# Kernel tuning notes

Hardware: AMD Instinct MI355X
Metric: run time of the kernel (lower is better)

## Reference

```python
import jax, jax.numpy as jnp
import numpy as np

B, S, D, H = 2, 4096, 512, 8
DH = D // H

def setup_inputs() -> dict:
    key = jax.random.key(0)
    k_enc, kq, kk, kv, ko = jax.random.split(key, 5)
    xavier = float(np.sqrt(6.0 / (D + D)))
    enc = jax.random.normal(k_enc, (B, S, D), dtype=jnp.float32)
    W_Q = jax.random.uniform(kq, (D, D), jnp.float32, -xavier, xavier)
    W_K = jax.random.uniform(kk, (D, D), jnp.float32, -xavier, xavier)
    W_V = jax.random.uniform(kv, (D, D), jnp.float32, -xavier, xavier)
    W_O = jax.random.uniform(ko, (D, D), jnp.float32, -xavier, xavier)
    # lower-triangular causal mask, broadcast over batch and heads
    causal_mask = jnp.tril(jnp.ones((S, S), dtype=jnp.int32))[None, None]
    return {"enc": enc, "causal_mask": causal_mask,
            "W_Q": W_Q, "W_K": W_K, "W_V": W_V, "W_O": W_O}

def reference(enc, causal_mask, W_Q, W_K, W_V, W_O):
    b, s, _ = enc.shape
    q = (enc @ W_Q).reshape(b, s, H, DH).transpose(0, 2, 1, 3)  # [b,h,s,dh]
    k = (enc @ W_K).reshape(b, s, H, DH).transpose(0, 2, 1, 3)
    v = (enc @ W_V).reshape(b, s, H, DH).transpose(0, 2, 1, 3)
    scores = jnp.einsum('bhqd,bhkd->bhqk', q, k) / jnp.sqrt(jnp.float32(DH))
    scores = jnp.where(causal_mask == 0, -jnp.inf, scores)
    attn = jax.nn.softmax(scores, axis=-1)
    out = jnp.einsum('bhqk,bhkd->bhqd', attn, v)  # [b,h,s,dh]
    concat = out.transpose(0, 2, 1, 3).reshape(b, s, H * DH)
    return concat @ W_O
```

## Files before the change

kernel.cpp:

```cpp
#include <hip/hip_runtime.h>


typedef _Float16 f16x8 __attribute__((ext_vector_type(8)));
typedef float f32x16 __attribute__((ext_vector_type(16)));

__device__ __forceinline__ f32x16 mma32(f16x8 a, f16x8 b, f32x16 c) {
  return __builtin_amdgcn_mfma_f32_32x32x16_f16(a, b, c, 0, 0, 0);
}

__device__ __forceinline__ void gload16(const void* g, void* l) {
  __builtin_amdgcn_global_load_lds((const __attribute__((address_space(1))) void*)g,
                                   (__attribute__((address_space(3))) void*)l, 16, 0, 0);
}

__global__ __launch_bounds__(256) void prep_k(const float* __restrict__ enc,
                                              const float* __restrict__ WQ,
                                              const float* __restrict__ WK,
                                              const float* __restrict__ WV,
                                              const float* __restrict__ WO,
                                              _Float16* __restrict__ enc16,
                                              _Float16* __restrict__ WtQ,
                                              _Float16* __restrict__ WtK,
                                              _Float16* __restrict__ WtV,
                                              _Float16* __restrict__ WtO) {
  const int bid = blockIdx.x;
  if (bid < 2048) {
    const size_t i = (size_t)bid * 256 + threadIdx.x;
    const float4* p = (const float4*)(enc + i * 8);
    const float4 a = p[0], b = p[1];
    union { f16x8 v; uint4 u; } r;
    r.v[0] = (_Float16)a.x; r.v[1] = (_Float16)a.y; r.v[2] = (_Float16)a.z; r.v[3] = (_Float16)a.w;
    r.v[4] = (_Float16)b.x; r.v[5] = (_Float16)b.y; r.v[6] = (_Float16)b.z; r.v[7] = (_Float16)b.w;
    *(uint4*)(enc16 + i * 8) = r.u;
  } else {
    const int t = bid - 2048;
    const int wsel = t >> 8;
    const float* W = (wsel == 0) ? WQ : (wsel == 1) ? WK : (wsel == 2) ? WV : WO;
    _Float16* T = (wsel == 0) ? WtQ : (wsel == 1) ? WtK : (wsel == 2) ? WtV : WtO;
    const int tb = t & 255;
    const int k0 = (tb & 15) * 32, n0 = (tb >> 4) * 32;
    __shared__ float tt[32][33];
    const int c = threadIdx.x & 31, r8 = threadIdx.x >> 5;
#pragma unroll
    for (int p = 0; p < 4; ++p) tt[c][r8 + 8 * p] = W[(size_t)(k0 + r8 + 8 * p) * 512 + n0 + c];
    __syncthreads();
#pragma unroll
    for (int p = 0; p < 4; ++p)
      T[(size_t)(n0 + r8 + 8 * p) * 512 + k0 + c] = (_Float16)tt[r8 + 8 * p][c];
  }
}

__device__ __forceinline__ void gemm_core(const _Float16* __restrict__ A,
                                          const _Float16* __restrict__ Wt,
                                          int m0, int n0,
                                          _Float16* Al, _Float16* Bl,
                                          f32x16 acc[2][2]) {
  const int tid = threadIdx.x, w = tid >> 6, l = tid & 63;
  const int hi = l >> 5, li = l & 31;
  const int wm = w >> 1, wn = w & 1;
  const int srow = l >> 3, sunit = (l & 7) ^ (l >> 3);
  const int arow = 32 * w;

#pragma unroll
  for (int mb = 0; mb < 2; ++mb)
#pragma unroll
    for (int nb = 0; nb < 2; ++nb)
#pragma unroll
      for (int r = 0; r < 16; ++r) acc[mb][nb][r] = 0.f;

#pragma unroll
  for (int i = 0; i < 4; ++i) {
    gload16(A + (size_t)(m0 + arow + 8 * i + srow) * 512 + sunit * 8, Al + (arow + 8 * i) * 64);
    gload16(Wt + (size_t)(n0 + arow + 8 * i + srow) * 512 + sunit * 8, Bl + (arow + 8 * i) * 64);
  }
  for (int kk = 0; kk < 8; ++kk) {
    const int cur = kk & 1;
    __syncthreads();
    if (kk < 7) {
      const int kn = (kk + 1) * 64;
#pragma unroll
      for (int i = 0; i < 4; ++i) {
        gload16(A + (size_t)(m0 + arow + 8 * i + srow) * 512 + kn + sunit * 8,
                Al + (cur ^ 1) * 8192 + (arow + 8 * i) * 64);
        gload16(Wt + (size_t)(n0 + arow + 8 * i + srow) * 512 + kn + sunit * 8,
                Bl + (cur ^ 1) * 8192 + (arow + 8 * i) * 64);
      }
    }
#pragma unroll
    for (int ks = 0; ks < 4; ++ks) {
      f16x8 af[2], bf[2];
#pragma unroll
      for (int mb = 0; mb < 2; ++mb)
        af[mb] = *(const f16x8*)((const char*)(Al + cur * 8192 + (64 * wm + 32 * mb + li) * 64) +
                                 (((2 * ks + hi) ^ (li & 7)) << 4));
#pragma unroll
      for (int nb = 0; nb < 2; ++nb)
        bf[nb] = *(const f16x8*)((const char*)(Bl + cur * 8192 + (64 * wn + 32 * nb + li) * 64) +
                                 (((2 * ks + hi) ^ (li & 7)) << 4));
#pragma unroll
      for (int mb = 0; mb < 2; ++mb)
#pragma unroll
        for (int nb = 0; nb < 2; ++nb) acc[mb][nb] = mma32(af[mb], bf[nb], acc[mb][nb]);
    }
  }
}

__global__ __launch_bounds__(256) void qkv_k(const _Float16* __restrict__ A,
                                             const _Float16* __restrict__ WtQ,
                                             const _Float16* __restrict__ WtK,
                                             const _Float16* __restrict__ WtV,
                                             _Float16* __restrict__ Qw,
                                             _Float16* __restrict__ Kw,
                                             _Float16* __restrict__ Vpw,
                                             float qscale) {
  __shared__ __align__(16) _Float16 Al[2 * 128 * 64];
  __shared__ __align__(16) _Float16 Bl[2 * 128 * 64];
  const int m0 = blockIdx.x * 128;
  const int wid = blockIdx.y >> 2, n0 = (blockIdx.y & 3) * 128;
  const _Float16* Wt = (wid == 0) ? WtQ : (wid == 1) ? WtK : WtV;
  f32x16 acc[2][2];
  gemm_core(A, Wt, m0, n0, Al, Bl, acc);

  const int tid = threadIdx.x, w = tid >> 6, l = tid & 63;
  const int hi = l >> 5, li = l & 31;
  const int wm = w >> 1, wn = w & 1;
  if (wid < 2) {
    _Float16* Cp = (wid == 0) ? Qw : Kw;
    const float scale = (wid == 0) ? qscale : 1.f;
#pragma unroll
    for (int mb = 0; mb < 2; ++mb)
#pragma unroll
      for (int nb = 0; nb < 2; ++nb)
#pragma unroll
        for (int r = 0; r < 16; ++r) {
          const int m = m0 + 64 * wm + 32 * mb + (r & 3) + 8 * (r >> 2) + 4 * hi;
          const int n = n0 + 64 * wn + 32 * nb + li;
          const int b = m >> 12, s = m & 4095, h = n >> 6, d = n & 63;
          Cp[((((size_t)b * 8 + h) * 4096 + s) << 6) + d] = (_Float16)(acc[mb][nb][r] * scale);
        }
  } else {
#pragma unroll
    for (int mb = 0; mb < 2; ++mb)
#pragma unroll
      for (int nb = 0; nb < 2; ++nb)
#pragma unroll
        for (int c = 0; c < 4; ++c) {
          const int mbase = m0 + 64 * wm + 32 * mb + 16 * (c >> 1);
          const int n = n0 + 64 * wn + 32 * nb + li;
          const int b = mbase >> 12, sb = mbase & 4095, h = n >> 6, d = n & 63;
          union { uint2 u; _Float16 h4[4]; } t4;
#pragma unroll
          for (int t = 0; t < 4; ++t) t4.h4[t] = (_Float16)acc[mb][nb][4 * c + t];
          *(uint2*)(Vpw + ((((size_t)b * 8 + h) * 64 + d) << 12) + sb + 4 * (c & 1) + 8 * hi) = t4.u;
        }
  }
}

__global__ __launch_bounds__(256) void fgemm_k(const _Float16* __restrict__ A,
                                               const _Float16* __restrict__ Wt,
                                               float* __restrict__ out) {
  __shared__ __align__(16) _Float16 Al[2 * 128 * 64];
  __shared__ __align__(16) _Float16 Bl[2 * 128 * 64];
  const int m0 = blockIdx.x * 128, n0 = blockIdx.y * 128;
  f32x16 acc[2][2];
  gemm_core(A, Wt, m0, n0, Al, Bl, acc);
  const int tid = threadIdx.x, w = tid >> 6, l = tid & 63;
  const int hi = l >> 5, li = l & 31;
  const int wm = w >> 1, wn = w & 1;
#pragma unroll
  for (int mb = 0; mb < 2; ++mb)
#pragma unroll
    for (int nb = 0; nb < 2; ++nb)
#pragma unroll
      for (int r = 0; r < 16; ++r) {
        const int m = m0 + 64 * wm + 32 * mb + (r & 3) + 8 * (r >> 2) + 4 * hi;
        const int n = n0 + 64 * wn + 32 * nb + li;
        out[(size_t)m * 512 + n] = acc[mb][nb][r];
      }
}

__global__ __launch_bounds__(128) void flash_k(const _Float16* __restrict__ Q,
                                               const _Float16* __restrict__ K,
                                               const _Float16* __restrict__ Vp,
                                               _Float16* __restrict__ att,
                                               _Float16* __restrict__ pO,
                                               float2* __restrict__ ml) {
  __shared__ __align__(16) _Float16 Kl[2 * 64 * 64];
  __shared__ __align__(16) _Float16 Vl[2 * 64 * 64];

  const int u = blockIdx.x;
  const int bh = u & 15;
  const int j = u >> 4;
  int qt, ktlo, kthi, cc;
  if (j < 32) {
    qt = 32 + j; ktlo = 0; kthi = 31; cc = 0;
  } else {
    const int i = (j - 32) >> 1;
    qt = ((j - 32) & 1) ? 63 - i : 31 - i;
    ktlo = (qt >= 32) ? 32 : 0;
    kthi = qt; cc = 1;
  }
  const bool split = (qt >= 32);
  const int q0 = qt * 64;
  const int tid = threadIdx.x, w = tid >> 6, l = tid & 63;
  const int hi = l >> 5, li = l & 31;
  const int srow = l >> 3, sunit = (l & 7) ^ (l >> 3);

  const size_t bhoff = (size_t)bh * 4096 * 64;
  const _Float16* Kb = K + bhoff;
  const _Float16* Vb = Vp + bhoff;
  const _Float16* Qb = Q + bhoff;
  const int qg = q0 + 32 * w + li;

  f16x8 qB[4];
#pragma unroll
  for (int ks = 0; ks < 4; ++ks)
    qB[ks] = *(const f16x8*)(Qb + (size_t)qg * 64 + 16 * ks + 8 * hi);

  f32x16 o2[2], lacc;
#pragma unroll
  for (int db = 0; db < 2; ++db)
#pragma unroll
    for (int r = 0; r < 16; ++r) o2[db][r] = 0.f;
#pragma unroll
  for (int r = 0; r < 16; ++r) lacc[r] = 0.f;
  float m_ = -__builtin_inff();

#pragma unroll
  for (int e = 0; e < 4; ++e) {
    const int row = 32 * w + 8 * e;
    gload16(Kb + (size_t)(ktlo * 64 + row + srow) * 64 + sunit * 8, Kl + row * 64);
    gload16(Vb + (size_t)(row + srow) * 4096 + ktlo * 64 + sunit * 8, Vl + row * 64);
  }

  for (int kt = ktlo; kt <= kthi; ++kt) {
    const int cur = kt & 1;
    __syncthreads();
    if (kt < kthi) {
      const int k0n = (kt + 1) * 64;
#pragma unroll
      for (int e = 0; e < 4; ++e) {
        const int row = 32 * w + 8 * e;
        gload16(Kb + (size_t)(k0n + row + srow) * 64 + sunit * 8,
                Kl + (cur ^ 1) * 4096 + row * 64);
        gload16(Vb + (size_t)(row + srow) * 4096 + k0n + sunit * 8,
                Vl + (cur ^ 1) * 4096 + row * 64);
      }
    }

    f32x16 s2[2];
#pragma unroll
    for (int kb = 0; kb < 2; ++kb)
#pragma unroll
      for (int r = 0; r < 16; ++r) s2[kb][r] = 0.f;
    __builtin_amdgcn_s_setprio(1);
#pragma unroll
    for (int ks = 0; ks < 4; ++ks)
#pragma unroll
      for (int kb = 0; kb < 2; ++kb) {
        const f16x8 kf = *(const f16x8*)((const char*)(Kl + cur * 4096 + (32 * kb + li) * 64) +
                                         (((2 * ks + hi) ^ (li & 7)) << 4));
        s2[kb] = mma32(kf, qB[ks], s2[kb]);
      }
    __builtin_amdgcn_s_setprio(0);

    if (kt == qt) {
      const int limit = 32 * w + li;
#pragma unroll
      for (int kb = 0; kb < 2; ++kb)
#pragma unroll
        for (int r = 0; r < 16; ++r) {
          const int kl = 32 * kb + (r & 3) + 8 * (r >> 2) + 4 * hi;
          if (kl > limit) s2[kb][r] = -__builtin_inff();
        }
    }

#define RV(i) s2[(i) >> 4][(i) & 15]
    float a[11];
#pragma unroll
    for (int i = 0; i < 10; ++i)
      a[i] = fmaxf(fmaxf(RV(3 * i), RV(3 * i + 1)), RV(3 * i + 2));
    a[10] = fmaxf(RV(30), RV(31));
#undef RV
    float b4[4];
    b4[0] = fmaxf(fmaxf(a[0], a[1]), a[2]);
    b4[1] = fmaxf(fmaxf(a[3], a[4]), a[5]);
    b4[2] = fmaxf(fmaxf(a[6], a[7]), a[8]);
    b4[3] = fmaxf(a[9], a[10]);
    const float mxl = fmaxf(fmaxf(fmaxf(b4[0], b4[1]), b4[2]), b4[3]);

    if (!__all(mxl <= m_ + 8.f)) {
      const float vm = fmaxf(mxl, __shfl_xor(mxl, 32, 64));
      const float mn = fmaxf(m_, vm);
      const float al = __builtin_amdgcn_exp2f(m_ - mn);
      m_ = mn;
#pragma unroll
      for (int r = 0; r < 16; ++r) lacc[r] *= al;
#pragma unroll
      for (int db = 0; db < 2; ++db)
#pragma unroll
        for (int r = 0; r < 16; ++r) o2[db][r] *= al;
    }
#pragma unroll
    for (int kb = 0; kb < 2; ++kb)
#pragma unroll
      for (int r = 0; r < 16; ++r) s2[kb][r] = __builtin_amdgcn_exp2f(s2[kb][r] - m_);
#pragma unroll
    for (int kb = 0; kb < 2; ++kb)
#pragma unroll
      for (int r = 0; r < 16; ++r) lacc[r] += s2[kb][r];

    f16x8 pb[4];
#pragma unroll
    for (int ks = 0; ks < 4; ++ks) {
      union { f16x8 v; unsigned int u[4]; } pu;
      const int kb = ks >> 1, base = 8 * (ks & 1);
#pragma unroll
      for (int p2 = 0; p2 < 4; ++p2)
        pu.u[p2] = __builtin_bit_cast(unsigned int,
                     __builtin_amdgcn_cvt_pkrtz(s2[kb][base + 2 * p2], s2[kb][base + 2 * p2 + 1]));
      pb[ks] = pu.v;
    }

    __builtin_amdgcn_s_setprio(1);
#pragma unroll
    for (int ks = 0; ks < 4; ++ks)
#pragma unroll
      for (int db = 0; db < 2; ++db) {
        const f16x8 vf = *(const f16x8*)((const char*)(Vl + cur * 4096 + (32 * db + li) * 64) +
                                         (((2 * ks + hi) ^ (li & 7)) << 4));
        o2[db] = mma32(vf, pb[ks], o2[db]);
      }
    __builtin_amdgcn_s_setprio(0);
  }

  float t8[8];
#pragma unroll
  for (int i = 0; i < 8; ++i) t8[i] = lacc[i] + lacc[i + 8];
  float lsum = ((t8[0] + t8[1]) + (t8[2] + t8[3])) + ((t8[4] + t8[5]) + (t8[6] + t8[7]));
  lsum += __shfl_xor(lsum, 32, 64);
  const float inv = 1.f / lsum;
  if (!split) {
    const int b = bh >> 3, h = bh & 7;
    _Float16* op = att + ((size_t)b * 4096 + qg) * 512 + h * 64;
#pragma unroll
    for (int db = 0; db < 2; ++db)
#pragma unroll
      for (int c = 0; c < 4; ++c) {
        union { uint2 u; _Float16 h4[4]; } t4;
#pragma unroll
        for (int t = 0; t < 4; ++t) t4.h4[t] = (_Float16)(o2[db][4 * c + t] * inv);
        *(uint2*)(op + 32 * db + 8 * c + 4 * hi) = t4.u;
      }
  } else {
    const int slot = (bh * 32 + (qt - 32)) * 2 + cc;
    const int qrow = 32 * w + li;
    _Float16* op = pO + (size_t)slot * 4096 + qrow * 64;
#pragma unroll
    for (int db = 0; db < 2; ++db)
#pragma unroll
      for (int c = 0; c < 4; ++c) {
        union { uint2 u; _Float16 h4[4]; } t4;
#pragma unroll
        for (int t = 0; t < 4; ++t) t4.h4[t] = (_Float16)(o2[db][4 * c + t] * inv);
        *(uint2*)(op + 32 * db + 8 * c + 4 * hi) = t4.u;
      }
    if (hi == 0) ml[slot * 64 + qrow] = make_float2(m_, lsum);
  }
}

__global__ __launch_bounds__(256) void combine_k(const float2* __restrict__ ml,
                                                 const _Float16* __restrict__ pO,
                                                 _Float16* __restrict__ att) {
  const int tid = threadIdx.x;
  const int rid = blockIdx.x * 8 + (tid >> 5);
  const int d2 = tid & 31;
  const int bh = rid >> 11, rem = rid & 2047;
  const int qm = rem >> 6, qrow = rem & 63;
  const int slot0 = (bh * 32 + qm) * 2;
  const float2 ml0 = ml[slot0 * 64 + qrow];
  const float2 ml1 = ml[slot0 * 64 + 64 + qrow];
  const float M = fmaxf(ml0.x, ml1.x);
  const float w0 = __builtin_amdgcn_exp2f(ml0.x - M) * ml0.y;
  const float w1 = __builtin_amdgcn_exp2f(ml1.x - M) * ml1.y;
  const float inv = 1.f / (w0 + w1);
  const float a0 = w0 * inv, a1 = w1 * inv;
  union { unsigned int u; _Float16 h2[2]; } x0, x1, y;
  x0.u = *(const unsigned int*)(pO + (size_t)slot0 * 4096 + qrow * 64 + 2 * d2);
  x1.u = *(const unsigned int*)(pO + (size_t)(slot0 + 1) * 4096 + qrow * 64 + 2 * d2);
  y.h2[0] = (_Float16)((float)x0.h2[0] * a0 + (float)x1.h2[0] * a1);
  y.h2[1] = (_Float16)((float)x0.h2[1] * a0 + (float)x1.h2[1] * a1);
  const int b = bh >> 3, h = bh & 7, q = (32 + qm) * 64 + qrow;
  *(unsigned int*)(att + ((size_t)b * 4096 + q) * 512 + h * 64 + 2 * d2) = y.u;
}

extern "C" void kernel_launch(void* const* d_in, const int* in_sizes, int n_in,
                              void* d_out, int out_size, void* d_ws, size_t ws_size,
                              hipStream_t stream) {
  const float* enc = (const float*)d_in[0];
  const float* WQ = (const float*)d_in[2];
  const float* WK = (const float*)d_in[3];
  const float* WV = (const float*)d_in[4];
  const float* WO = (const float*)d_in[5];
  float* out = (float*)d_out;

  const size_t NE = (size_t)2 * 8 * 4096 * 64;
  _Float16* enc16 = (_Float16*)d_ws;
  _Float16* pO = enc16;
  _Float16* Qw = enc16 + NE;
  _Float16* Kw = Qw + NE;
  _Float16* Vpw = Kw + NE;
  _Float16* WtQ = Vpw + NE;
  _Float16* WtK = WtQ + 512 * 512;
  _Float16* WtV = WtK + 512 * 512;
  _Float16* WtO = WtV + 512 * 512;
  _Float16* att = WtO + 512 * 512;
  float2* ml = (float2*)WtQ;

  prep_k<<<3072, 256, 0, stream>>>(enc, WQ, WK, WV, WO, enc16, WtQ, WtK, WtV, WtO);
  qkv_k<<<dim3(64, 12), 256, 0, stream>>>(enc16, WtQ, WtK, WtV, Qw, Kw, Vpw, 0.1803368801f);
  flash_k<<<1536, 128, 0, stream>>>(Qw, Kw, Vpw, att, pO, ml);
  combine_k<<<4096, 256, 0, stream>>>(ml, pO, att);
  fgemm_k<<<dim3(64, 4), 256, 0, stream>>>(att, WtO, out);
}
```

Before: 111.9 us.

## Split causal flash attention into 20-tile KV chunks with heaviest-first scheduling

Replaces the two-way KV split of upper query tiles with chunks of up to 20 key tiles, so long query tiles are split into 2-4 partial blocks and the grid grows from 1536 to 2176 blocks, issued in reverse order so the largest work starts first. The combine kernel is generalised to merge a variable number of partials with log-sum-exp weights. Partial outputs are moved into the output buffer and the row statistics into the enc16 workspace to make room for more slots. This aims to even out per-block work and reduce tail imbalance, at the cost of more partial writes and combine traffic.

```diff
diff --git a/kernel.cpp b/kernel.cpp
--- a/kernel.cpp
+++ b/kernel.cpp
@@ -190,17 +190,15 @@
 
   const int u = blockIdx.x;
   const int bh = u & 15;
-  const int j = u >> 4;
-  int qt, ktlo, kthi, cc;
-  if (j < 32) {
-    qt = 32 + j; ktlo = 0; kthi = 31; cc = 0;
-  } else {
-    const int i = (j - 32) >> 1;
-    qt = ((j - 32) & 1) ? 63 - i : 31 - i;
-    ktlo = (qt >= 32) ? 32 : 0;
-    kthi = qt; cc = 1;
-  }
-  const bool split = (qt >= 32);
+  const int j = 135 - (u >> 4);
+  int qt, cc;
+  if (j < 20) { qt = j; cc = 0; }
+  else if (j < 60) { qt = 20 + ((j - 20) >> 1); cc = (j - 20) & 1; }
+  else if (j < 120) { qt = 40 + (j - 60) / 3; cc = (j - 60) % 3; }
+  else { qt = 60 + ((j - 120) >> 2); cc = (j - 120) & 3; }
+  const int ktlo = 20 * cc;
+  const int kthi = min(20 * cc + 19, qt);
+  const bool split = (qt >= 20);
   const int q0 = qt * 64;
   const int tid = threadIdx.x, w = tid >> 6, l = tid & 63;
   const int hi = l >> 5, li = l & 31;
@@ -353,7 +351,11 @@
         *(uint2*)(op + 32 * db + 8 * c + 4 * hi) = t4.u;
       }
   } else {
-    const int slot = (bh * 32 + (qt - 32)) * 2 + cc;
+    int off;
+    if (qt < 40) off = (qt - 20) * 2;
+    else if (qt < 60) off = 40 + (qt - 40) * 3;
+    else off = 100 + (qt - 60) * 4;
+    const int slot = bh * 116 + off + cc;
     const int qrow = 32 * w + li;
     _Float16* op = pO + (size_t)slot * 4096 + qrow * 64;
 #pragma unroll
@@ -375,22 +377,45 @@
   const int tid = threadIdx.x;
   const int rid = blockIdx.x * 8 + (tid >> 5);
   const int d2 = tid & 31;
-  const int bh = rid >> 11, rem = rid & 2047;
-  const int qm = rem >> 6, qrow = rem & 63;
-  const int slot0 = (bh * 32 + qm) * 2;
-  const float2 ml0 = ml[slot0 * 64 + qrow];
-  const float2 ml1 = ml[slot0 * 64 + 64 + qrow];
-  const float M = fmaxf(ml0.x, ml1.x);
-  const float w0 = __builtin_amdgcn_exp2f(ml0.x - M) * ml0.y;
-  const float w1 = __builtin_amdgcn_exp2f(ml1.x - M) * ml1.y;
-  const float inv = 1.f / (w0 + w1);
-  const float a0 = w0 * inv, a1 = w1 * inv;
-  union { unsigned int u; _Float16 h2[2]; } x0, x1, y;
-  x0.u = *(const unsigned int*)(pO + (size_t)slot0 * 4096 + qrow * 64 + 2 * d2);
-  x1.u = *(const unsigned int*)(pO + (size_t)(slot0 + 1) * 4096 + qrow * 64 + 2 * d2);
-  y.h2[0] = (_Float16)((float)x0.h2[0] * a0 + (float)x1.h2[0] * a1);
-  y.h2[1] = (_Float16)((float)x0.h2[1] * a0 + (float)x1.h2[1] * a1);
-  const int b = bh >> 3, h = bh & 7, q = (32 + qm) * 64 + qrow;
+  const int bh = rid / 2816, rem = rid % 2816;
+  const int qt = 20 + (rem >> 6), qrow = rem & 63;
+  const int nc = (qt + 20) / 20;
+  int off;
+  if (qt < 40) off = (qt - 20) * 2;
+  else if (qt < 60) off = 40 + (qt - 40) * 3;
+  else off = 100 + (qt - 60) * 4;
+  const int slot0 = bh * 116 + off;
+
+  float2 mlc[4];
+  float M = -__builtin_inff();
+#pragma unroll
+  for (int c = 0; c < 4; ++c)
+    if (c < nc) {
+      mlc[c] = ml[(slot0 + c) * 64 + qrow];
+      M = fmaxf(M, mlc[c].x);
+    }
+  float wc[4], wsum = 0.f;
+#pragma unroll
+  for (int c = 0; c < 4; ++c)
+    if (c < nc) {
+      wc[c] = __builtin_amdgcn_exp2f(mlc[c].x - M) * mlc[c].y;
+      wsum += wc[c];
+    }
+  const float inv = 1.f / wsum;
+  float acc0 = 0.f, acc1 = 0.f;
+#pragma unroll
+  for (int c = 0; c < 4; ++c)
+    if (c < nc) {
+      union { unsigned int u; _Float16 h2[2]; } x;
+      x.u = *(const unsigned int*)(pO + (size_t)(slot0 + c) * 4096 + qrow * 64 + 2 * d2);
+      const float a = wc[c] * inv;
+      acc0 += (float)x.h2[0] * a;
+      acc1 += (float)x.h2[1] * a;
+    }
+  union { unsigned int u; _Float16 h2[2]; } y;
+  y.h2[0] = (_Float16)acc0;
+  y.h2[1] = (_Float16)acc1;
+  const int b = bh >> 3, h = bh & 7, q = qt * 64 + qrow;
   *(unsigned int*)(att + ((size_t)b * 4096 + q) * 512 + h * 64 + 2 * d2) = y.u;
 }
 
@@ -406,7 +431,6 @@
 
   const size_t NE = (size_t)2 * 8 * 4096 * 64;
   _Float16* enc16 = (_Float16*)d_ws;
-  _Float16* pO = enc16;
   _Float16* Qw = enc16 + NE;
   _Float16* Kw = Qw + NE;
   _Float16* Vpw = Kw + NE;
@@ -415,11 +439,12 @@
   _Float16* WtV = WtK + 512 * 512;
   _Float16* WtO = WtV + 512 * 512;
   _Float16* att = WtO + 512 * 512;
-  float2* ml = (float2*)WtQ;
+  float2* ml = (float2*)enc16;
+  _Float16* pO = (_Float16*)d_out;
 
   prep_k<<<3072, 256, 0, stream>>>(enc, WQ, WK, WV, WO, enc16, WtQ, WtK, WtV, WtO);
   qkv_k<<<dim3(64, 12), 256, 0, stream>>>(enc16, WtQ, WtK, WtV, Qw, Kw, Vpw, 0.1803368801f);
-  flash_k<<<1536, 128, 0, stream>>>(Qw, Kw, Vpw, att, pO, ml);
-  combine_k<<<4096, 256, 0, stream>>>(ml, pO, att);
+  flash_k<<<2176, 128, 0, stream>>>(Qw, Kw, Vpw, att, pO, ml);
+  combine_k<<<5632, 256, 0, stream>>>(ml, pO, att);
   fgemm_k<<<dim3(64, 4), 256, 0, stream>>>(att, WtO, out);
 }
```

Measured after the change: 128.0 us. 1.14x slower.

## Load K/V in 128-key pairs per barrier, dropping double-buffer prefetch

Applied to the files above, without the earlier changes.

The flash attention kernel now loads two 64-key K/V tiles at once into a single 128-key LDS buffer, with a new swizzle for the wider V rows. It then processes both tiles between barriers. This halves the number of barrier rounds per key range. However, it removes the prefetch of the next tile that overlapped with compute, so every load is now exposed and waited on before any math runs.

```diff
diff --git a/kernel.cpp b/kernel.cpp
--- a/kernel.cpp
+++ b/kernel.cpp
@@ -185,8 +185,8 @@
                                                _Float16* __restrict__ att,
                                                _Float16* __restrict__ pO,
                                                float2* __restrict__ ml) {
-  __shared__ __align__(16) _Float16 Kl[2 * 64 * 64];
-  __shared__ __align__(16) _Float16 Vl[2 * 64 * 64];
+  __shared__ __align__(16) _Float16 Kl[128 * 64];
+  __shared__ __align__(16) _Float16 Vl[64 * 128];
 
   const int u = blockIdx.x;
   const int bh = u & 15;
@@ -204,7 +204,6 @@
   const int q0 = qt * 64;
   const int tid = threadIdx.x, w = tid >> 6, l = tid & 63;
   const int hi = l >> 5, li = l & 31;
-  const int srow = l >> 3, sunit = (l & 7) ^ (l >> 3);
 
   const size_t bhoff = (size_t)bh * 4096 * 64;
   const _Float16* Kb = K + bhoff;
@@ -226,28 +225,7 @@
   for (int r = 0; r < 16; ++r) lacc[r] = 0.f;
   float m_ = -__builtin_inff();
 
-#pragma unroll
-  for (int e = 0; e < 4; ++e) {
-    const int row = 32 * w + 8 * e;
-    gload16(Kb + (size_t)(ktlo * 64 + row + srow) * 64 + sunit * 8, Kl + row * 64);
-    gload16(Vb + (size_t)(row + srow) * 4096 + ktlo * 64 + sunit * 8, Vl + row * 64);
-  }
-
-  for (int kt = ktlo; kt <= kthi; ++kt) {
-    const int cur = kt & 1;
-    __syncthreads();
-    if (kt < kthi) {
-      const int k0n = (kt + 1) * 64;
-#pragma unroll
-      for (int e = 0; e < 4; ++e) {
-        const int row = 32 * w + 8 * e;
-        gload16(Kb + (size_t)(k0n + row + srow) * 64 + sunit * 8,
-                Kl + (cur ^ 1) * 4096 + row * 64);
-        gload16(Vb + (size_t)(row + srow) * 4096 + k0n + sunit * 8,
-                Vl + (cur ^ 1) * 4096 + row * 64);
-      }
-    }
-
+  auto tile_step = [&](int kt, int half) {
     f32x16 s2[2];
 #pragma unroll
     for (int kb = 0; kb < 2; ++kb)
@@ -258,8 +236,9 @@
     for (int ks = 0; ks < 4; ++ks)
 #pragma unroll
       for (int kb = 0; kb < 2; ++kb) {
-        const f16x8 kf = *(const f16x8*)((const char*)(Kl + cur * 4096 + (32 * kb + li) * 64) +
-                                         (((2 * ks + hi) ^ (li & 7)) << 4));
+        const f16x8 kf = *(const f16x8*)(
+            (const char*)(Kl + (64 * half + 32 * kb + li) * 64) +
+            (((2 * ks + hi) ^ (li & 7)) << 4));
         s2[kb] = mma32(kf, qB[ks], s2[kb]);
       }
     __builtin_amdgcn_s_setprio(0);
@@ -327,11 +306,36 @@
     for (int ks = 0; ks < 4; ++ks)
 #pragma unroll
       for (int db = 0; db < 2; ++db) {
-        const f16x8 vf = *(const f16x8*)((const char*)(Vl + cur * 4096 + (32 * db + li) * 64) +
-                                         (((2 * ks + hi) ^ (li & 7)) << 4));
+        const f16x8 vf = *(const f16x8*)(
+            (const char*)(Vl + (32 * db + li) * 128) +
+            ((((8 * half + 2 * ks + hi)) ^ (li & 15)) << 4));
         o2[db] = mma32(vf, pb[ks], o2[db]);
       }
     __builtin_amdgcn_s_setprio(0);
+  };
+
+  const int npair = (kthi - ktlo + 2) >> 1;
+  for (int p = 0; p < npair; ++p) {
+    const int kt0 = ktlo + 2 * p;
+    const int k0 = kt0 * 64;
+    if (p) __syncthreads();
+#pragma unroll
+    for (int e = 0; e < 8; ++e) {
+      const int kr = 64 * w + 8 * e;
+      gload16(Kb + (size_t)(k0 + kr + (l >> 3)) * 64 + (((l & 7) ^ ((l >> 3) & 7)) << 3),
+              Kl + kr * 64);
+    }
+#pragma unroll
+    for (int e = 0; e < 8; ++e) {
+      const int vr = 32 * w + 4 * e;
+      gload16(Vb + (size_t)(vr + (l >> 4)) * 4096 + k0 +
+                  ((((l & 15) ^ ((4 * e + (l >> 4)) & 15))) << 3),
+              Vl + vr * 128);
+    }
+    __syncthreads();
+
+    tile_step(kt0, 0);
+    if (kt0 + 1 <= kthi) tile_step(kt0 + 1, 1);
   }
 
   float t8[8];
```

After: 111.2 us, median of 2. About the same (-0.6%).
